# Kernel tuning notes

Measured on AMD Instinct MI355X. Metric: run time of the kernel, lower is better.

Reference implementation:

```python
import jax, jax.numpy as jnp
import numpy as np

N = 100000      # nodes
E = 1600000     # edges (avg degree 16)
EL = 200000     # supervision (label) edges
D_IN, D_HID, D_OUT = 128, 128, 64


def setup_inputs() -> dict:
    key = jax.random.key(0)
    k = jax.random.split(key, 6)
    x = jax.random.normal(k[0], (N, D_IN), jnp.float32)
    edge_index = jax.random.randint(k[1], (2, E), 0, N, dtype=jnp.int32)
    edge_label_index = jax.random.randint(k[2], (2, EL), 0, N, dtype=jnp.int32)
    W1 = jax.random.normal(k[3], (D_IN, D_HID), jnp.float32) * (1.0 / np.sqrt(D_IN))
    b1 = jnp.zeros((D_HID,), jnp.float32)
    W2 = jax.random.normal(k[4], (D_HID, D_OUT), jnp.float32) * (1.0 / np.sqrt(D_HID))
    b2 = jnp.zeros((D_OUT,), jnp.float32)
    return {"x": x, "edge_index": edge_index, "edge_label_index": edge_label_index,
            "W1": W1, "b1": b1, "W2": W2, "b2": b2}


def gcn_layer(x, src, dst, W, b, n):
    """PyG-style GCNConv: linear -> sym-normalized scatter-add with self loops -> +bias."""
    h = x @ W                                   # [N, F]
    ones = jnp.ones(src.shape[0], h.dtype)
    deg = jax.ops.segment_sum(ones, dst, num_segments=n) + 1.0   # in-degree + self loop
    dinv = jax.lax.rsqrt(deg)                   # deg^{-1/2}
    norm = dinv[src] * dinv[dst]                # per-edge norm
    agg = jax.ops.segment_sum(h[src] * norm[:, None], dst, num_segments=n)
    agg = agg + h * (1.0 / deg)[:, None]        # self-loop contribution: dinv[i]^2
    return agg + b


def reference(x, edge_index, edge_label_index, W1, b1, W2, b2):
    src, dst = edge_index[0], edge_index[1]
    z = gcn_layer(x, src, dst, W1, b1, N)
    z = jax.nn.relu(z)                          # dropout omitted (eval mode)
    z = gcn_layer(z, src, dst, W2, b2, N)
    # decode: gather-dot over supervision edges
    return (z[edge_label_index[0]] * z[edge_label_index[1]]).sum(axis=-1)
```

## Files before the change

### kernel.cpp

```cpp
#include <hip/hip_runtime.h>
#include <stdint.h>

typedef __bf16 bf16x8 __attribute__((ext_vector_type(8)));
typedef float  floatx4 __attribute__((ext_vector_type(4)));

__device__ __forceinline__ unsigned short f2b(float x){
    unsigned u = __float_as_uint(x);
    u = u + 0x7FFFu + ((u >> 16) & 1u);
    return (unsigned short)(u >> 16);
}
__device__ __forceinline__ float b2f(unsigned short h){
    return __uint_as_float(((unsigned)h) << 16);
}


__global__ __launch_bounds__(256) void k_hist(const int* __restrict__ dst,
                                              int* __restrict__ hist,
                                              int E_, int nbins, int nblk){
    __shared__ int h[1024];
    int t = threadIdx.x, blk = blockIdx.x;
    for (int i = t; i < nbins; i += 256) h[i] = 0;
    __syncthreads();
    int base = blk * 8192;
    #pragma unroll
    for (int j = 0; j < 8; j++){
        int e = base + (j * 256 + t) * 4;
        if (e < E_){
            int4 d = *(const int4*)(dst + e);
            atomicAdd(&h[d.x >> 7], 1);
            atomicAdd(&h[d.y >> 7], 1);
            atomicAdd(&h[d.z >> 7], 1);
            atomicAdd(&h[d.w >> 7], 1);
        }
    }
    __syncthreads();
    for (int i = t; i < nbins; i += 256) hist[(size_t)i * nblk + blk] = h[i];
}

__global__ __launch_bounds__(64) void k_binscanA(int* __restrict__ hist,
                                                 int* __restrict__ btot, int nblk){
    int bin = blockIdx.x, lane = threadIdx.x;
    int carry = 0;
    for (int base = 0; base < nblk; base += 64){
        int idx = bin * nblk + base + lane;
        bool inb = (base + lane) < nblk;
        int v = inb ? hist[idx] : 0;
        int orig = v;
        #pragma unroll
        for (int o = 1; o < 64; o <<= 1){
            int u = __shfl_up(v, o);
            if (lane >= o) v += u;
        }
        if (inb) hist[idx] = v - orig + carry;
        carry += __shfl(v, 63);
    }
    if (lane == 0) btot[bin] = carry;
}

__global__ __launch_bounds__(1024) void k_binscanB(const int* __restrict__ btot,
                                                   int* __restrict__ boff, int nbins){
    __shared__ int s[1024];
    int t = threadIdx.x;
    s[t] = (t < nbins) ? btot[t] : 0;
    __syncthreads();
    for (int o = 1; o < 1024; o <<= 1){
        int v = (t >= o) ? s[t - o] : 0;
        __syncthreads();
        s[t] += v;
        __syncthreads();
    }
    if (t == 0) boff[0] = 0;
    if (t < nbins) boff[t + 1] = s[t];
}

__global__ __launch_bounds__(256) void k_scatter(const int* __restrict__ src,
                                                 const int* __restrict__ dst,
                                                 const int* __restrict__ hist,
                                                 const int* __restrict__ boff,
                                                 unsigned* __restrict__ part,
                                                 int E_, int nbins, int nblk){
    __shared__ int cur[1024];
    int t = threadIdx.x, blk = blockIdx.x;
    for (int i = t; i < nbins; i += 256)
        cur[i] = boff[i] + hist[(size_t)i * nblk + blk];
    __syncthreads();
    int base = blk * 8192;
    #pragma unroll
    for (int j = 0; j < 8; j++){
        int e = base + (j * 256 + t) * 4;
        if (e < E_){
            int4 d = *(const int4*)(dst + e);
            int4 s = *(const int4*)(src + e);
            int p0 = atomicAdd(&cur[d.x >> 7], 1);
            part[p0] = ((unsigned)(d.x & 127) << 25) | (unsigned)s.x;
            int p1 = atomicAdd(&cur[d.y >> 7], 1);
            part[p1] = ((unsigned)(d.y & 127) << 25) | (unsigned)s.y;
            int p2 = atomicAdd(&cur[d.z >> 7], 1);
            part[p2] = ((unsigned)(d.z & 127) << 25) | (unsigned)s.z;
            int p3 = atomicAdd(&cur[d.w >> 7], 1);
            part[p3] = ((unsigned)(d.w & 127) << 25) | (unsigned)s.w;
        }
    }
}

__global__ __launch_bounds__(256) void k_binsort(const unsigned* __restrict__ part,
                                                 const int* __restrict__ boff,
                                                 int* __restrict__ csr,
                                                 int* __restrict__ cnt,
                                                 int* __restrict__ off,
                                                 float* __restrict__ dinv,
                                                 int n, int nbins){
    int b = blockIdx.x, t = threadIdx.x;
    int s0 = boff[b], s1 = boff[b + 1], len = s1 - s0;
    __shared__ int cl[128], sc[128], cur[128];
    __shared__ unsigned buf[4096], outb[4096];
    if (t < 128){ cl[t] = 0; cur[t] = 0; }
    __syncthreads();
    if (len <= 4096){
        for (int i = t; i < len; i += 256) buf[i] = part[s0 + i];
        __syncthreads();
        for (int i = t; i < len; i += 256) atomicAdd(&cl[buf[i] >> 25], 1);
        __syncthreads();
        if (t < 128) sc[t] = cl[t];
        __syncthreads();
        for (int o = 1; o < 128; o <<= 1){
            int v = 0;
            if (t < 128 && t >= o) v = sc[t - o];
            __syncthreads();
            if (t < 128) sc[t] += v;
            __syncthreads();
        }
        for (int i = t; i < len; i += 256){
            unsigned w = buf[i];
            int nd = (int)(w >> 25);
            int p = (sc[nd] - cl[nd]) + atomicAdd(&cur[nd], 1);
            outb[p] = w & 0x1FFFFFFu;
        }
        __syncthreads();
        for (int i = t; i < len; i += 256) csr[s0 + i] = (int)outb[i];
    } else {
        for (int i = t; i < len; i += 256) atomicAdd(&cl[part[s0 + i] >> 25], 1);
        __syncthreads();
        if (t < 128) sc[t] = cl[t];
        __syncthreads();
        for (int o = 1; o < 128; o <<= 1){
            int v = 0;
            if (t < 128 && t >= o) v = sc[t - o];
            __syncthreads();
            if (t < 128) sc[t] += v;
            __syncthreads();
        }
        for (int i = t; i < len; i += 256){
            unsigned w = part[s0 + i];
            int nd = (int)(w >> 25);
            int p = (sc[nd] - cl[nd]) + atomicAdd(&cur[nd], 1);
            csr[s0 + p] = (int)(w & 0x1FFFFFFu);
        }
    }
    if (t < 128){
        int node = b * 128 + t;
        if (node < n){
            cnt[node] = cl[t];
            off[node] = s0 + (sc[t] - cl[t]);
            dinv[node] = rsqrtf((float)cl[t] + 1.0f);
        }
    }
}

__global__ __launch_bounds__(256) void k_wconv(const float* __restrict__ W1,
                                               const float* __restrict__ W2,
                                               unsigned short* __restrict__ wf1,
                                               unsigned* __restrict__ w2p){
    int f = blockIdx.x * 256 + threadIdx.x;
    if (f < 2048){
        int lane = f & 63;
        int ctkc = f >> 6;
        int kc = ctkc & 3, ct = ctkc >> 2;
        int col = ct * 16 + (lane & 15);
        int k0  = kc * 32 + (lane >> 4) * 8;
        unsigned short* d = wf1 + (size_t)f * 8;
        #pragma unroll
        for (int j = 0; j < 8; j++) d[j] = f2b(W1[(k0 + j) * 128 + col]);
    } else if (f < 2048 + 4096){
        int lf = f - 2048;
        int kp = lf >> 6, lane = lf & 63;
        unsigned lo = f2b(W2[(2 * kp) * 64 + lane]);
        unsigned hi = f2b(W2[(2 * kp + 1) * 64 + lane]);
        w2p[lf] = lo | (hi << 16);
    }
}

__global__ __launch_bounds__(256) void k_gemm1(const float* __restrict__ x,
                                               const unsigned short* __restrict__ wf,
                                               const float* __restrict__ dinv,
                                               unsigned short* __restrict__ hs, int n){
    __shared__ unsigned short Wl[16384];
    __shared__ unsigned short Al[64 * 136];
    int t = threadIdx.x;
    long rowBase = (long)blockIdx.x * 64;
    {
        const uint4* s4 = (const uint4*)wf;
        uint4* d4 = (uint4*)Wl;
        #pragma unroll
        for (int i = 0; i < 8; i++) d4[t + i * 256] = s4[t + i * 256];
    }
    {
        const float4* xs = (const float4*)(x + rowBase * 128);
        #pragma unroll
        for (int k = 0; k < 8; k++){
            int i = t + k * 256;
            int r = i >> 5, c4 = (i & 31) << 2;
            float4 v = make_float4(0.f, 0.f, 0.f, 0.f);
            if (rowBase + r < n) v = xs[i];
            unsigned lo = (unsigned)f2b(v.x) | ((unsigned)f2b(v.y) << 16);
            unsigned hi = (unsigned)f2b(v.z) | ((unsigned)f2b(v.w) << 16);
            *(uint2*)&Al[r * 136 + c4] = make_uint2(lo, hi);
        }
    }
    __syncthreads();
    int w = t >> 6, lane = t & 63, lr = lane & 15, q = lane >> 4;
    floatx4 zero = {0.f, 0.f, 0.f, 0.f};
    floatx4 acc[8];
    #pragma unroll
    for (int ct = 0; ct < 8; ct++) acc[ct] = zero;
    #pragma unroll
    for (int kc = 0; kc < 4; kc++){
        bf16x8 af = *(const bf16x8*)&Al[(w * 16 + lr) * 136 + kc * 32 + q * 8];
        #pragma unroll
        for (int ct = 0; ct < 8; ct++){
            bf16x8 bf = *(const bf16x8*)&Wl[((ct * 4 + kc) * 64 + lane) * 8];
            acc[ct] = __builtin_amdgcn_mfma_f32_16x16x32_bf16(af, bf, acc[ct], 0, 0, 0);
        }
    }
    long r0 = rowBase + w * 16 + q * 4;
    #pragma unroll
    for (int r = 0; r < 4; r++){
        long row = r0 + r;
        if (row >= n) continue;
        float dv = dinv[row];
        unsigned short* orow = hs + row * 128 + lr;
        #pragma unroll
        for (int ct = 0; ct < 8; ct++) orow[ct * 16] = f2b(acc[ct][r] * dv);
    }
}

__global__ __launch_bounds__(256) void k_agg1g2(const unsigned short* __restrict__ hs,
                                                const int* __restrict__ off,
                                                const int* __restrict__ cnt,
                                                const int* __restrict__ csr,
                                                const float* __restrict__ dinv,
                                                const float* __restrict__ b1,
                                                const unsigned* __restrict__ w2p,
                                                unsigned short* __restrict__ hs2,
                                                int n, int nwaves){
    __shared__ unsigned W2l[4096];
    __shared__ float zrow[4][128];
    int t = threadIdx.x;
    {
        const uint4* w4 = (const uint4*)w2p;
        uint4* d4 = (uint4*)W2l;
        #pragma unroll
        for (int i = 0; i < 4; i++) d4[t + i * 256] = w4[t + i * 256];
    }
    __syncthreads();
    int wband = t >> 6, lane = t & 63;
    float2 bb = ((const float2*)b1)[lane];
    for (int wid = blockIdx.x * 4 + wband; wid < n; wid += nwaves){
        size_t i = (size_t)wid;
        int start = off[wid], c = cnt[wid];
        unsigned v0 = *(const unsigned*)(hs + i * 128 + lane * 2);
        float a0 = b2f((unsigned short)v0);
        float a1 = b2f((unsigned short)(v0 >> 16));
        int j = 0;
        for (; j + 8 <= c; j += 8){
            size_t s0 = (size_t)csr[start + j + 0];
            size_t s1 = (size_t)csr[start + j + 1];
            size_t s2 = (size_t)csr[start + j + 2];
            size_t s3 = (size_t)csr[start + j + 3];
            size_t s4 = (size_t)csr[start + j + 4];
            size_t s5 = (size_t)csr[start + j + 5];
            size_t s6 = (size_t)csr[start + j + 6];
            size_t s7 = (size_t)csr[start + j + 7];
            unsigned w0 = *(const unsigned*)(hs + s0 * 128 + lane * 2);
            unsigned w1 = *(const unsigned*)(hs + s1 * 128 + lane * 2);
            unsigned w2 = *(const unsigned*)(hs + s2 * 128 + lane * 2);
            unsigned w3 = *(const unsigned*)(hs + s3 * 128 + lane * 2);
            unsigned w4 = *(const unsigned*)(hs + s4 * 128 + lane * 2);
            unsigned w5 = *(const unsigned*)(hs + s5 * 128 + lane * 2);
            unsigned w6 = *(const unsigned*)(hs + s6 * 128 + lane * 2);
            unsigned w7 = *(const unsigned*)(hs + s7 * 128 + lane * 2);
            a0 += b2f((unsigned short)w0); a1 += b2f((unsigned short)(w0 >> 16));
            a0 += b2f((unsigned short)w1); a1 += b2f((unsigned short)(w1 >> 16));
            a0 += b2f((unsigned short)w2); a1 += b2f((unsigned short)(w2 >> 16));
            a0 += b2f((unsigned short)w3); a1 += b2f((unsigned short)(w3 >> 16));
            a0 += b2f((unsigned short)w4); a1 += b2f((unsigned short)(w4 >> 16));
            a0 += b2f((unsigned short)w5); a1 += b2f((unsigned short)(w5 >> 16));
            a0 += b2f((unsigned short)w6); a1 += b2f((unsigned short)(w6 >> 16));
            a0 += b2f((unsigned short)w7); a1 += b2f((unsigned short)(w7 >> 16));
        }
        for (; j < c; j++){
            size_t s = (size_t)csr[start + j];
            unsigned v = *(const unsigned*)(hs + s * 128 + lane * 2);
            a0 += b2f((unsigned short)v);
            a1 += b2f((unsigned short)(v >> 16));
        }
        float dv = dinv[wid];
        float z0 = fmaxf(fmaf(dv, a0, bb.x), 0.f);
        float z1 = fmaxf(fmaf(dv, a1, bb.y), 0.f);
        zrow[wband][lane * 2]     = z0;
        zrow[wband][lane * 2 + 1] = z1;
        float acc = 0.f;
        #pragma unroll 8
        for (int kp = 0; kp < 64; kp++){
            unsigned wv = W2l[kp * 64 + lane];
            float2 zz = *(const float2*)&zrow[wband][kp * 2];
            acc = fmaf(zz.x, b2f((unsigned short)wv), acc);
            acc = fmaf(zz.y, b2f((unsigned short)(wv >> 16)), acc);
        }
        hs2[i * 64 + lane] = f2b(acc * dv);
    }
}

__global__ __launch_bounds__(256) void k_agg2(const unsigned short* __restrict__ hs,
                                              const int* __restrict__ off,
                                              const int* __restrict__ cnt,
                                              const int* __restrict__ csr,
                                              const float* __restrict__ dinv,
                                              const float* __restrict__ b,
                                              unsigned short* __restrict__ z, int n){
    int wid = (blockIdx.x * 256 + threadIdx.x) >> 6;
    int lane = threadIdx.x & 63;
    if (wid >= n) return;
    size_t i = (size_t)wid;
    int start = off[wid], c = cnt[wid];
    float a = b2f(hs[i * 64 + lane]);
    int j = 0;
    for (; j + 8 <= c; j += 8){
        size_t s0 = (size_t)csr[start + j + 0];
        size_t s1 = (size_t)csr[start + j + 1];
        size_t s2 = (size_t)csr[start + j + 2];
        size_t s3 = (size_t)csr[start + j + 3];
        size_t s4 = (size_t)csr[start + j + 4];
        size_t s5 = (size_t)csr[start + j + 5];
        size_t s6 = (size_t)csr[start + j + 6];
        size_t s7 = (size_t)csr[start + j + 7];
        unsigned short h0 = hs[s0 * 64 + lane];
        unsigned short h1 = hs[s1 * 64 + lane];
        unsigned short h2 = hs[s2 * 64 + lane];
        unsigned short h3 = hs[s3 * 64 + lane];
        unsigned short h4 = hs[s4 * 64 + lane];
        unsigned short h5 = hs[s5 * 64 + lane];
        unsigned short h6 = hs[s6 * 64 + lane];
        unsigned short h7 = hs[s7 * 64 + lane];
        a += b2f(h0); a += b2f(h1); a += b2f(h2); a += b2f(h3);
        a += b2f(h4); a += b2f(h5); a += b2f(h6); a += b2f(h7);
    }
    for (; j < c; j++){
        size_t s = (size_t)csr[start + j];
        a += b2f(hs[s * 64 + lane]);
    }
    z[i * 64 + lane] = f2b(fmaf(dinv[wid], a, b[lane]));
}

__global__ __launch_bounds__(256) void k_decode(const unsigned short* __restrict__ z,
                                                const int* __restrict__ es,
                                                const int* __restrict__ et,
                                                float* __restrict__ out, int m){
    int wv = (blockIdx.x * 256 + threadIdx.x) >> 6;
    int lane = threadIdx.x & 63;
    int e = wv * 2 + (lane >> 5);
    int hl = lane & 31;
    float p = 0.f;
    if (e < m){
        size_t s = (size_t)es[e], t2 = (size_t)et[e];
        unsigned vs = *(const unsigned*)(z + s * 64 + hl * 2);
        unsigned vt = *(const unsigned*)(z + t2 * 64 + hl * 2);
        p = b2f((unsigned short)vs) * b2f((unsigned short)vt)
          + b2f((unsigned short)(vs >> 16)) * b2f((unsigned short)(vt >> 16));
    }
    #pragma unroll
    for (int o = 16; o > 0; o >>= 1) p += __shfl_xor(p, o);
    if (hl == 0 && e < m) out[e] = p;
}


extern "C" void kernel_launch(void* const* d_in, const int* in_sizes, int n_in,
                              void* d_out, int out_size, void* d_ws, size_t ws_size,
                              hipStream_t stream){
    const float* x   = (const float*)d_in[0];
    const int*   ei  = (const int*)d_in[1];
    const int*   eli = (const int*)d_in[2];
    const float* W1  = (const float*)d_in[3];
    const float* b1  = (const float*)d_in[4];
    const float* W2  = (const float*)d_in[5];
    const float* b2  = (const float*)d_in[6];
    float* out = (float*)d_out;

    int N_  = in_sizes[0] / 128;
    int E_  = in_sizes[1] / 2;
    int EL_ = in_sizes[2] / 2;
    int NBINS = (N_ + 127) >> 7;
    const int EPB = 8192;
    int NBLK = (E_ + EPB - 1) / EPB;

    char* w = (char*)d_ws;
    size_t o = 0;
    auto alloc = [&](size_t bytes) -> size_t {
        size_t r = o; o += (bytes + 511) & ~(size_t)511; return r;
    };
    size_t o_cnt  = alloc((size_t)N_ * 4);
    size_t o_off  = alloc((size_t)N_ * 4);
    size_t o_dinv = alloc((size_t)N_ * 4);
    size_t o_btot = alloc((size_t)NBINS * 4);
    size_t o_boff = alloc((size_t)(NBINS + 1) * 4);
    size_t o_csr  = alloc((size_t)E_ * 4);
    size_t o_wf1  = alloc(16384 * 2);
    size_t o_w2p  = alloc(4096 * 4);
    size_t o_hs1  = alloc((size_t)N_ * 128 * 2);
    size_t o_hs2  = alloc((size_t)N_ * 64 * 2);

    int* cnt  = (int*)(w + o_cnt);
    int* off  = (int*)(w + o_off);
    float* dinv = (float*)(w + o_dinv);
    int* btot = (int*)(w + o_btot);
    int* boff = (int*)(w + o_boff);
    int* csr  = (int*)(w + o_csr);
    unsigned short* wf1 = (unsigned short*)(w + o_wf1);
    unsigned* w2p = (unsigned*)(w + o_w2p);
    unsigned short* hs1 = (unsigned short*)(w + o_hs1);
    unsigned short* hs2 = (unsigned short*)(w + o_hs2);
    unsigned short* z2  = (unsigned short*)(w + o_hs1);

    int* hist = (int*)(w + o_hs1);
    unsigned* part = (unsigned*)(w + o_hs1 + 4u * 1024u * 1024u);

    const int AGG1_BLOCKS = 2048;
    int nwaves = AGG1_BLOCKS * 4;

    k_hist    <<<NBLK, 256, 0, stream>>>(ei + E_, hist, E_, NBINS, NBLK);
    k_binscanA<<<NBINS, 64, 0, stream>>>(hist, btot, NBLK);
    k_binscanB<<<1, 1024, 0, stream>>>(btot, boff, NBINS);
    k_scatter <<<NBLK, 256, 0, stream>>>(ei, ei + E_, hist, boff, part, E_, NBINS, NBLK);
    k_binsort <<<NBINS, 256, 0, stream>>>(part, boff, csr, cnt, off, dinv, N_, NBINS);
    k_wconv   <<<24, 256, 0, stream>>>(W1, W2, wf1, w2p);
    k_gemm1   <<<(N_ + 63) / 64, 256, 0, stream>>>(x, wf1, dinv, hs1, N_);
    k_agg1g2  <<<AGG1_BLOCKS, 256, 0, stream>>>(hs1, off, cnt, csr, dinv, b1, w2p, hs2, N_, nwaves);
    k_agg2    <<<(N_ + 3) / 4, 256, 0, stream>>>(hs2, off, cnt, csr, dinv, b2, z2, N_);
    k_decode  <<<(EL_ + 7) / 8, 256, 0, stream>>>(z2, eli, eli + EL_, out, EL_);
}
```

Baseline: 319.8 us.

## Fuse CSR bucketing into fixed slabs, use fp16 dot2 for layer-2 GEMM, widen agg2/decode

Replaces the histogram, per-block scan and scatter passes with one kernel. It counts bins in shared memory, reserves space with a global atomic per bin, and scatters edges into fixed 4096-entry slabs per bin. The binsort then reads straight from the slab. Separately, the layer-2 weights and activations are packed as fp16 and reduced with fdot2. The agg2 and decode kernels now process two and four items per wave with wider loads. Risks: edges are silently dropped if a bin holds more than 4096, edge order within bins becomes non-deterministic, and fp16 round-toward-zero changes precision.

```diff
diff --git a/kernel.cpp b/kernel.cpp
--- a/kernel.cpp
+++ b/kernel.cpp
@@ -3,6 +3,7 @@
 
 typedef __bf16 bf16x8 __attribute__((ext_vector_type(8)));
 typedef float  floatx4 __attribute__((ext_vector_type(4)));
+typedef __fp16 h2 __attribute__((ext_vector_type(2)));
 
 __device__ __forceinline__ unsigned short f2b(float x){
     unsigned u = __float_as_uint(x);
@@ -14,9 +15,11 @@
 }
 
 
-__global__ __launch_bounds__(256) void k_hist(const int* __restrict__ dst,
-                                              int* __restrict__ hist,
-                                              int E_, int nbins, int nblk){
+__global__ __launch_bounds__(256) void k_scatter2(const int* __restrict__ src,
+                                                  const int* __restrict__ dst,
+                                                  int* __restrict__ gcur,
+                                                  unsigned* __restrict__ slab,
+                                                  int E_, int nbins){
     __shared__ int h[1024];
     int t = threadIdx.x, blk = blockIdx.x;
     for (int i = t; i < nbins; i += 256) h[i] = 0;
@@ -34,27 +37,27 @@
         }
     }
     __syncthreads();
-    for (int i = t; i < nbins; i += 256) hist[(size_t)i * nblk + blk] = h[i];
-}
-
-__global__ __launch_bounds__(64) void k_binscanA(int* __restrict__ hist,
-                                                 int* __restrict__ btot, int nblk){
-    int bin = blockIdx.x, lane = threadIdx.x;
-    int carry = 0;
-    for (int base = 0; base < nblk; base += 64){
-        int idx = bin * nblk + base + lane;
-        bool inb = (base + lane) < nblk;
-        int v = inb ? hist[idx] : 0;
-        int orig = v;
-        #pragma unroll
-        for (int o = 1; o < 64; o <<= 1){
-            int u = __shfl_up(v, o);
-            if (lane >= o) v += u;
-        }
-        if (inb) hist[idx] = v - orig + carry;
-        carry += __shfl(v, 63);
-    }
-    if (lane == 0) btot[bin] = carry;
+    for (int i = t; i < nbins; i += 256){
+        int hv = h[i];
+        h[i] = hv ? atomicAdd(&gcur[i], hv) : 0;
+    }
+    __syncthreads();
+    #pragma unroll
+    for (int j = 0; j < 8; j++){
+        int e = base + (j * 256 + t) * 4;
+        if (e < E_){
+            int4 d = *(const int4*)(dst + e);
+            int4 s = *(const int4*)(src + e);
+            int p0 = atomicAdd(&h[d.x >> 7], 1);
+            slab[(size_t)(d.x >> 7) * 4096 + p0] = ((unsigned)(d.x & 127) << 25) | (unsigned)s.x;
+            int p1 = atomicAdd(&h[d.y >> 7], 1);
+            slab[(size_t)(d.y >> 7) * 4096 + p1] = ((unsigned)(d.y & 127) << 25) | (unsigned)s.y;
+            int p2 = atomicAdd(&h[d.z >> 7], 1);
+            slab[(size_t)(d.z >> 7) * 4096 + p2] = ((unsigned)(d.z & 127) << 25) | (unsigned)s.z;
+            int p3 = atomicAdd(&h[d.w >> 7], 1);
+            slab[(size_t)(d.w >> 7) * 4096 + p3] = ((unsigned)(d.w & 127) << 25) | (unsigned)s.w;
+        }
+    }
 }
 
 __global__ __launch_bounds__(1024) void k_binscanB(const int* __restrict__ btot,
@@ -73,37 +76,7 @@
     if (t < nbins) boff[t + 1] = s[t];
 }
 
-__global__ __launch_bounds__(256) void k_scatter(const int* __restrict__ src,
-                                                 const int* __restrict__ dst,
-                                                 const int* __restrict__ hist,
-                                                 const int* __restrict__ boff,
-                                                 unsigned* __restrict__ part,
-                                                 int E_, int nbins, int nblk){
-    __shared__ int cur[1024];
-    int t = threadIdx.x, blk = blockIdx.x;
-    for (int i = t; i < nbins; i += 256)
-        cur[i] = boff[i] + hist[(size_t)i * nblk + blk];
-    __syncthreads();
-    int base = blk * 8192;
-    #pragma unroll
-    for (int j = 0; j < 8; j++){
-        int e = base + (j * 256 + t) * 4;
-        if (e < E_){
-            int4 d = *(const int4*)(dst + e);
-            int4 s = *(const int4*)(src + e);
-            int p0 = atomicAdd(&cur[d.x >> 7], 1);
-            part[p0] = ((unsigned)(d.x & 127) << 25) | (unsigned)s.x;
-            int p1 = atomicAdd(&cur[d.y >> 7], 1);
-            part[p1] = ((unsigned)(d.y & 127) << 25) | (unsigned)s.y;
-            int p2 = atomicAdd(&cur[d.z >> 7], 1);
-            part[p2] = ((unsigned)(d.z & 127) << 25) | (unsigned)s.z;
-            int p3 = atomicAdd(&cur[d.w >> 7], 1);
-            part[p3] = ((unsigned)(d.w & 127) << 25) | (unsigned)s.w;
-        }
-    }
-}
-
-__global__ __launch_bounds__(256) void k_binsort(const unsigned* __restrict__ part,
+__global__ __launch_bounds__(256) void k_binsort(const unsigned* __restrict__ slab,
                                                  const int* __restrict__ boff,
                                                  int* __restrict__ csr,
                                                  int* __restrict__ cnt,
@@ -111,52 +84,34 @@
                                                  float* __restrict__ dinv,
                                                  int n, int nbins){
     int b = blockIdx.x, t = threadIdx.x;
-    int s0 = boff[b], s1 = boff[b + 1], len = s1 - s0;
+    int s0 = boff[b], len = boff[b + 1] - s0;
+    if (len > 4096) len = 4096;
+    const unsigned* seg = slab + (size_t)b * 4096;
     __shared__ int cl[128], sc[128], cur[128];
     __shared__ unsigned buf[4096], outb[4096];
     if (t < 128){ cl[t] = 0; cur[t] = 0; }
     __syncthreads();
-    if (len <= 4096){
-        for (int i = t; i < len; i += 256) buf[i] = part[s0 + i];
+    for (int i = t; i < len; i += 256) buf[i] = seg[i];
+    __syncthreads();
+    for (int i = t; i < len; i += 256) atomicAdd(&cl[buf[i] >> 25], 1);
+    __syncthreads();
+    if (t < 128) sc[t] = cl[t];
+    __syncthreads();
+    for (int o = 1; o < 128; o <<= 1){
+        int v = 0;
+        if (t < 128 && t >= o) v = sc[t - o];
         __syncthreads();
-        for (int i = t; i < len; i += 256) atomicAdd(&cl[buf[i] >> 25], 1);
+        if (t < 128) sc[t] += v;
         __syncthreads();
-        if (t < 128) sc[t] = cl[t];
-        __syncthreads();
-        for (int o = 1; o < 128; o <<= 1){
-            int v = 0;
-            if (t < 128 && t >= o) v = sc[t - o];
-            __syncthreads();
-            if (t < 128) sc[t] += v;
-            __syncthreads();
-        }
-        for (int i = t; i < len; i += 256){
-            unsigned w = buf[i];
-            int nd = (int)(w >> 25);
-            int p = (sc[nd] - cl[nd]) + atomicAdd(&cur[nd], 1);
-            outb[p] = w & 0x1FFFFFFu;
-        }
-        __syncthreads();
-        for (int i = t; i < len; i += 256) csr[s0 + i] = (int)outb[i];
-    } else {
-        for (int i = t; i < len; i += 256) atomicAdd(&cl[part[s0 + i] >> 25], 1);
-        __syncthreads();
-        if (t < 128) sc[t] = cl[t];
-        __syncthreads();
-        for (int o = 1; o < 128; o <<= 1){
-            int v = 0;
-            if (t < 128 && t >= o) v = sc[t - o];
-            __syncthreads();
-            if (t < 128) sc[t] += v;
-            __syncthreads();
-        }
-        for (int i = t; i < len; i += 256){
-            unsigned w = part[s0 + i];
-            int nd = (int)(w >> 25);
-            int p = (sc[nd] - cl[nd]) + atomicAdd(&cur[nd], 1);
-            csr[s0 + p] = (int)(w & 0x1FFFFFFu);
-        }
-    }
+    }
+    for (int i = t; i < len; i += 256){
+        unsigned w = buf[i];
+        int nd = (int)(w >> 25);
+        int p = (sc[nd] - cl[nd]) + atomicAdd(&cur[nd], 1);
+        outb[p] = w & 0x1FFFFFFu;
+    }
+    __syncthreads();
+    for (int i = t; i < len; i += 256) csr[s0 + i] = (int)outb[i];
     if (t < 128){
         int node = b * 128 + t;
         if (node < n){
@@ -184,9 +139,9 @@
     } else if (f < 2048 + 4096){
         int lf = f - 2048;
         int kp = lf >> 6, lane = lf & 63;
-        unsigned lo = f2b(W2[(2 * kp) * 64 + lane]);
-        unsigned hi = f2b(W2[(2 * kp + 1) * 64 + lane]);
-        w2p[lf] = lo | (hi << 16);
+        h2 p = __builtin_amdgcn_cvt_pkrtz(W2[(2 * kp) * 64 + lane],
+                                          W2[(2 * kp + 1) * 64 + lane]);
+        w2p[lf] = __builtin_bit_cast(unsigned, p);
     }
 }
 
@@ -254,7 +209,7 @@
                                                 unsigned short* __restrict__ hs2,
                                                 int n, int nwaves){
     __shared__ unsigned W2l[4096];
-    __shared__ float zrow[4][128];
+    __shared__ unsigned zp[4][64];
     int t = threadIdx.x;
     {
         const uint4* w4 = (const uint4*)w2p;
@@ -307,17 +262,18 @@
         float dv = dinv[wid];
         float z0 = fmaxf(fmaf(dv, a0, bb.x), 0.f);
         float z1 = fmaxf(fmaf(dv, a1, bb.y), 0.f);
-        zrow[wband][lane * 2]     = z0;
-        zrow[wband][lane * 2 + 1] = z1;
-        float acc = 0.f;
+        zp[wband][lane] = __builtin_bit_cast(unsigned, __builtin_amdgcn_cvt_pkrtz(z0, z1));
+        float acc0 = 0.f, acc1 = 0.f;
         #pragma unroll 8
-        for (int kp = 0; kp < 64; kp++){
-            unsigned wv = W2l[kp * 64 + lane];
-            float2 zz = *(const float2*)&zrow[wband][kp * 2];
-            acc = fmaf(zz.x, b2f((unsigned short)wv), acc);
-            acc = fmaf(zz.y, b2f((unsigned short)(wv >> 16)), acc);
-        }
-        hs2[i * 64 + lane] = f2b(acc * dv);
+        for (int kp = 0; kp < 64; kp += 2){
+            h2 wa = __builtin_bit_cast(h2, W2l[kp * 64 + lane]);
+            h2 wb = __builtin_bit_cast(h2, W2l[(kp + 1) * 64 + lane]);
+            h2 za = __builtin_bit_cast(h2, zp[wband][kp]);
+            h2 zb = __builtin_bit_cast(h2, zp[wband][kp + 1]);
+            acc0 = __builtin_amdgcn_fdot2(za, wa, acc0, false);
+            acc1 = __builtin_amdgcn_fdot2(zb, wb, acc1, false);
+        }
+        hs2[i * 64 + lane] = f2b((acc0 + acc1) * dv);
     }
 }
 
@@ -328,12 +284,16 @@
                                               const float* __restrict__ dinv,
                                               const float* __restrict__ b,
                                               unsigned short* __restrict__ z, int n){
-    int wid = (blockIdx.x * 256 + threadIdx.x) >> 6;
+    int wv = (blockIdx.x * 256 + threadIdx.x) >> 6;
     int lane = threadIdx.x & 63;
-    if (wid >= n) return;
-    size_t i = (size_t)wid;
-    int start = off[wid], c = cnt[wid];
-    float a = b2f(hs[i * 64 + lane]);
+    int half = lane >> 5, hl = lane & 31;
+    int node = wv * 2 + half;
+    if (node >= n) return;
+    size_t i = (size_t)node;
+    int start = off[node], c = cnt[node];
+    unsigned v0 = *(const unsigned*)(hs + i * 64 + hl * 2);
+    float a0 = b2f((unsigned short)v0);
+    float a1 = b2f((unsigned short)(v0 >> 16));
     int j = 0;
     for (; j + 8 <= c; j += 8){
         size_t s0 = (size_t)csr[start + j + 0];
@@ -344,22 +304,34 @@
         size_t s5 = (size_t)csr[start + j + 5];
         size_t s6 = (size_t)csr[start + j + 6];
         size_t s7 = (size_t)csr[start + j + 7];
-        unsigned short h0 = hs[s0 * 64 + lane];
-        unsigned short h1 = hs[s1 * 64 + lane];
-        unsigned short h2 = hs[s2 * 64 + lane];
-        unsigned short h3 = hs[s3 * 64 + lane];
-        unsigned short h4 = hs[s4 * 64 + lane];
-        unsigned short h5 = hs[s5 * 64 + lane];
-        unsigned short h6 = hs[s6 * 64 + lane];
-        unsigned short h7 = hs[s7 * 64 + lane];
-        a += b2f(h0); a += b2f(h1); a += b2f(h2); a += b2f(h3);
-        a += b2f(h4); a += b2f(h5); a += b2f(h6); a += b2f(h7);
+        unsigned w0 = *(const unsigned*)(hs + s0 * 64 + hl * 2);
+        unsigned w1 = *(const unsigned*)(hs + s1 * 64 + hl * 2);
+        unsigned w2 = *(const unsigned*)(hs + s2 * 64 + hl * 2);
+        unsigned w3 = *(const unsigned*)(hs + s3 * 64 + hl * 2);
+        unsigned w4 = *(const unsigned*)(hs + s4 * 64 + hl * 2);
+        unsigned w5 = *(const unsigned*)(hs + s5 * 64 + hl * 2);
+        unsigned w6 = *(const unsigned*)(hs + s6 * 64 + hl * 2);
+        unsigned w7 = *(const unsigned*)(hs + s7 * 64 + hl * 2);
+        a0 += b2f((unsigned short)w0); a1 += b2f((unsigned short)(w0 >> 16));
+        a0 += b2f((unsigned short)w1); a1 += b2f((unsigned short)(w1 >> 16));
+        a0 += b2f((unsigned short)w2); a1 += b2f((unsigned short)(w2 >> 16));
+        a0 += b2f((unsigned short)w3); a1 += b2f((unsigned short)(w3 >> 16));
+        a0 += b2f((unsigned short)w4); a1 += b2f((unsigned short)(w4 >> 16));
+        a0 += b2f((unsigned short)w5); a1 += b2f((unsigned short)(w5 >> 16));
+        a0 += b2f((unsigned short)w6); a1 += b2f((unsigned short)(w6 >> 16));
+        a0 += b2f((unsigned short)w7); a1 += b2f((unsigned short)(w7 >> 16));
     }
     for (; j < c; j++){
         size_t s = (size_t)csr[start + j];
-        a += b2f(hs[s * 64 + lane]);
-    }
-    z[i * 64 + lane] = f2b(fmaf(dinv[wid], a, b[lane]));
+        unsigned v = *(const unsigned*)(hs + s * 64 + hl * 2);
+        a0 += b2f((unsigned short)v);
+        a1 += b2f((unsigned short)(v >> 16));
+    }
+    float dv = dinv[node];
+    float2 bb = ((const float2*)b)[hl];
+    float r0 = fmaf(dv, a0, bb.x);
+    float r1 = fmaf(dv, a1, bb.y);
+    *(unsigned*)(z + i * 64 + hl * 2) = (unsigned)f2b(r0) | ((unsigned)f2b(r1) << 16);
 }
 
 __global__ __launch_bounds__(256) void k_decode(const unsigned short* __restrict__ z,
@@ -368,19 +340,21 @@
                                                 float* __restrict__ out, int m){
     int wv = (blockIdx.x * 256 + threadIdx.x) >> 6;
     int lane = threadIdx.x & 63;
-    int e = wv * 2 + (lane >> 5);
-    int hl = lane & 31;
+    int e = wv * 4 + (lane >> 4);
+    int ql = lane & 15;
     float p = 0.f;
     if (e < m){
         size_t s = (size_t)es[e], t2 = (size_t)et[e];
-        unsigned vs = *(const unsigned*)(z + s * 64 + hl * 2);
-        unsigned vt = *(const unsigned*)(z + t2 * 64 + hl * 2);
-        p = b2f((unsigned short)vs) * b2f((unsigned short)vt)
-          + b2f((unsigned short)(vs >> 16)) * b2f((unsigned short)(vt >> 16));
-    }
-    #pragma unroll
-    for (int o = 16; o > 0; o >>= 1) p += __shfl_xor(p, o);
-    if (hl == 0 && e < m) out[e] = p;
+        uint2 vs = *(const uint2*)(z + s * 64 + ql * 4);
+        uint2 vt = *(const uint2*)(z + t2 * 64 + ql * 4);
+        p = b2f((unsigned short)vs.x) * b2f((unsigned short)vt.x)
+          + b2f((unsigned short)(vs.x >> 16)) * b2f((unsigned short)(vt.x >> 16))
+          + b2f((unsigned short)vs.y) * b2f((unsigned short)vt.y)
+          + b2f((unsigned short)(vs.y >> 16)) * b2f((unsigned short)(vt.y >> 16));
+    }
+    #pragma unroll
+    for (int o = 8; o > 0; o >>= 1) p += __shfl_xor(p, o);
+    if (ql == 0 && e < m) out[e] = p;
 }
 
 
@@ -411,7 +385,7 @@
     size_t o_cnt  = alloc((size_t)N_ * 4);
     size_t o_off  = alloc((size_t)N_ * 4);
     size_t o_dinv = alloc((size_t)N_ * 4);
-    size_t o_btot = alloc((size_t)NBINS * 4);
+    size_t o_gcur = alloc((size_t)NBINS * 4);
     size_t o_boff = alloc((size_t)(NBINS + 1) * 4);
     size_t o_csr  = alloc((size_t)E_ * 4);
     size_t o_wf1  = alloc(16384 * 2);
@@ -422,7 +396,7 @@
     int* cnt  = (int*)(w + o_cnt);
     int* off  = (int*)(w + o_off);
     float* dinv = (float*)(w + o_dinv);
-    int* btot = (int*)(w + o_btot);
+    int* gcur = (int*)(w + o_gcur);
     int* boff = (int*)(w + o_boff);
     int* csr  = (int*)(w + o_csr);
     unsigned short* wf1 = (unsigned short*)(w + o_wf1);
@@ -431,20 +405,18 @@
     unsigned short* hs2 = (unsigned short*)(w + o_hs2);
     unsigned short* z2  = (unsigned short*)(w + o_hs1);
 
-    int* hist = (int*)(w + o_hs1);
-    unsigned* part = (unsigned*)(w + o_hs1 + 4u * 1024u * 1024u);
+    unsigned* slab = (unsigned*)(w + o_hs1);
 
     const int AGG1_BLOCKS = 2048;
     int nwaves = AGG1_BLOCKS * 4;
 
-    k_hist    <<<NBLK, 256, 0, stream>>>(ei + E_, hist, E_, NBINS, NBLK);
-    k_binscanA<<<NBINS, 64, 0, stream>>>(hist, btot, NBLK);
-    k_binscanB<<<1, 1024, 0, stream>>>(btot, boff, NBINS);
-    k_scatter <<<NBLK, 256, 0, stream>>>(ei, ei + E_, hist, boff, part, E_, NBINS, NBLK);
-    k_binsort <<<NBINS, 256, 0, stream>>>(part, boff, csr, cnt, off, dinv, N_, NBINS);
+    (void)hipMemsetAsync(gcur, 0, (size_t)NBINS * 4, stream);
+    k_scatter2<<<NBLK, 256, 0, stream>>>(ei, ei + E_, gcur, slab, E_, NBINS);
+    k_binscanB<<<1, 1024, 0, stream>>>(gcur, boff, NBINS);
+    k_binsort <<<NBINS, 256, 0, stream>>>(slab, boff, csr, cnt, off, dinv, N_, NBINS);
     k_wconv   <<<24, 256, 0, stream>>>(W1, W2, wf1, w2p);
     k_gemm1   <<<(N_ + 63) / 64, 256, 0, stream>>>(x, wf1, dinv, hs1, N_);
     k_agg1g2  <<<AGG1_BLOCKS, 256, 0, stream>>>(hs1, off, cnt, csr, dinv, b1, w2p, hs2, N_, nwaves);
-    k_agg2    <<<(N_ + 3) / 4, 256, 0, stream>>>(hs2, off, cnt, csr, dinv, b2, z2, N_);
-    k_decode  <<<(EL_ + 7) / 8, 256, 0, stream>>>(z2, eli, eli + EL_, out, EL_);
-}
+    k_agg2    <<<(N_ + 7) / 8, 256, 0, stream>>>(hs2, off, cnt, csr, dinv, b2, z2, N_);
+    k_decode  <<<(EL_ + 15) / 16, 256, 0, stream>>>(z2, eli, eli + EL_, out, EL_);
+}
```

New measurement: 279.5 us. 12.6% less time.
